# Kernel tuning notes

Hardware: AMD Instinct MI355X
Metric: run time of the kernel (lower is better)

Reference implementation:

```python
import jax, jax.numpy as jnp
import numpy as np
import math

D_MODEL = 1024
N_HEADS = 16
HEAD_DIM = D_MODEL // N_HEADS
PAD_INDEX = 0
NEG_INF = -1e9  # matches torch masked_fill value


def setup_inputs() -> dict:
    key = jax.random.key(0)
    ks = jax.random.split(key, 10)
    b, s = 2, 2048
    x = jax.random.normal(ks[0], (b, s, D_MODEL), dtype=jnp.float32)
    input_ids = jax.random.randint(ks[1], (b, s), 0, 32000, dtype=jnp.int64)
    scale = 1.0 / math.sqrt(D_MODEL)
    def lin(k):
        kw, kb = jax.random.split(k)
        W = jax.random.uniform(kw, (D_MODEL, D_MODEL), jnp.float32, -scale, scale)
        bb = jax.random.uniform(kb, (D_MODEL,), jnp.float32, -scale, scale)
        return W, bb
    Wq, bq = lin(ks[2])
    Wk, bk = lin(ks[3])
    Wv, bv = lin(ks[4])
    Wo, bo = lin(ks[5])
    return {"x": x, "input_ids": input_ids,
            "Wq": Wq, "bq": bq, "Wk": Wk, "bk": bk,
            "Wv": Wv, "bv": bv, "Wo": Wo, "bo": bo}


def reference(x, input_ids, Wq, bq, Wk, bk, Wv, bv, Wo, bo):
    b, s, _ = x.shape
    # torch nn.Linear: y = x @ W.T + b
    q = (x @ Wq.T + bq).reshape(b, s, N_HEADS, HEAD_DIM)
    k = (x @ Wk.T + bk).reshape(b, s, N_HEADS, HEAD_DIM)
    v = (x @ Wv.T + bv).reshape(b, s, N_HEADS, HEAD_DIM)
    # scores: [b, h, s, s]
    scores = jnp.einsum('bqhd,bkhd->bhqk', q, k) / math.sqrt(HEAD_DIM)
    pad_mask = (input_ids != PAD_INDEX)[:, None, None, :]          # [b,1,1,s] over keys
    causal = jnp.tril(jnp.ones((s, s), dtype=bool))[None, None]     # [1,1,s,s]
    final_mask = pad_mask & causal
    scores = jnp.where(final_mask, scores, NEG_INF)
    attn = jax.nn.softmax(scores, axis=-1)
    out = jnp.einsum('bhqk,bkhd->bqhd', attn, v).reshape(b, s, D_MODEL)
    return out @ Wo.T + bo
```

## Files before the change

kernel.cpp:

```cpp
#include <hip/hip_runtime.h>

#define DMODEL 1024
#define NHEADS 16
#define HDIM   64
#define BATCH  2
#define SEQ    2048
#define MROWS  (BATCH*SEQ)

typedef __bf16 bf16x8 __attribute__((ext_vector_type(8)));
typedef __bf16 bf16x4 __attribute__((ext_vector_type(4)));
typedef float floatx4 __attribute__((ext_vector_type(4)));

typedef const __attribute__((address_space(1))) void gvoid;
typedef __attribute__((address_space(3))) void lvoid;

template<bool V> struct ICb { static constexpr bool value = V; };

#define QSCALE 0.18033688011112042f

__global__ void cast_all(const float* __restrict__ x,
                         const float* __restrict__ wq, const float* __restrict__ wk,
                         const float* __restrict__ wv, const float* __restrict__ wo,
                         __bf16* __restrict__ xb, __bf16* __restrict__ wqb,
                         __bf16* __restrict__ wkb, __bf16* __restrict__ wvb,
                         __bf16* __restrict__ wob)
{
  const int u = blockIdx.x * 256 + threadIdx.x;
  const float* s; __bf16* o; int off;
  if (u < MROWS*DMODEL/8) { s = x; o = xb; off = u; }
  else {
    const int r = u - MROWS*DMODEL/8;
    const int w = r >> 17;
    off = r & 131071;
    s = (w == 0) ? wq : (w == 1) ? wk : (w == 2) ? wv : wo;
    o = (w == 0) ? wqb : (w == 1) ? wkb : (w == 2) ? wvb : wob;
  }
  const float4 f0 = ((const float4*)s)[off*2];
  const float4 f1 = ((const float4*)s)[off*2 + 1];
  bf16x8 v = {(__bf16)f0.x, (__bf16)f0.y, (__bf16)f0.z, (__bf16)f0.w,
              (__bf16)f1.x, (__bf16)f1.y, (__bf16)f1.z, (__bf16)f1.w};
  *(bf16x8*)(o + off*8) = v;
}

__global__ __launch_bounds__(256, 3)
void gemm_qkv(const unsigned short* __restrict__ A,
              const unsigned short* __restrict__ W0,
              const unsigned short* __restrict__ W1,
              const unsigned short* __restrict__ W2,
              const float* __restrict__ b0,
              const float* __restrict__ b1,
              const float* __restrict__ b2,
              unsigned short* __restrict__ qout,
              unsigned short* __restrict__ kout,
              unsigned short* __restrict__ vout)
{
  const int K = DMODEL;
  __shared__ unsigned short As[2][128*32];
  __shared__ unsigned short Bs[2][128*32];
  const int tid  = threadIdx.x;
  const int wid  = tid >> 6;
  const int lane = tid & 63;

  const int lin = blockIdx.x;
  const int wg  = (lin & 7)*96 + (lin >> 3);
  const int bx  = wg % 24;
  const int by  = wg / 24;
  const int brow = by * 128;
  const int bcol = bx * 128;
  const int wr = (wid >> 1) * 64;
  const int wc = (wid & 1) * 64;

  const int which = bcol >> 10;
  const unsigned short* Bw = which == 0 ? W0 : which == 1 ? W1 : W2;
  const float* bias = which == 0 ? b0 : which == 1 ? b1 : b2;
  const int bcolL = bcol & 1023;

  floatx4 acc[4][4] = {};

  const int sr = wid*16 + (lane >> 2);
  const int sc = (lane & 3) * 8;
  const int fr = lane & 15;
  const int fk = (lane >> 4) * 8;

#define GSTAGE(KT, B) do {                                                     \
    _Pragma("unroll")                                                          \
    for (int i_ = 0; i_ < 2; ++i_) {                                           \
      __builtin_amdgcn_global_load_lds(                                        \
          (gvoid*)(A + (size_t)(brow + i_*64 + sr)*K + (KT) + sc),             \
          (lvoid*)(As[B] + i_*2048 + wid*512), 16, 0, 0);                      \
      __builtin_amdgcn_global_load_lds(                                        \
          (gvoid*)(Bw + (size_t)(bcolL + i_*64 + sr)*K + (KT) + sc),           \
          (lvoid*)(Bs[B] + i_*2048 + wid*512), 16, 0, 0);                      \
    }                                                                          \
  } while (0)

  GSTAGE(0, 0);

  for (int kt = 0; kt < K; kt += 32) {
    const int cur = (kt >> 5) & 1;
    if (kt + 32 < K) {
      GSTAGE(kt + 32, cur ^ 1);
      asm volatile("s_waitcnt vmcnt(4)" ::: "memory");
    } else {
      asm volatile("s_waitcnt vmcnt(0)" ::: "memory");
    }
    __builtin_amdgcn_s_barrier();
    __builtin_amdgcn_sched_barrier(0);

    bf16x8 af[4], bfv[4];
#pragma unroll
    for (int m = 0; m < 4; ++m)
      af[m] = *(const bf16x8*)(As[cur] + (wr + m*16 + fr)*32 + fk);
#pragma unroll
    for (int n = 0; n < 4; ++n)
      bfv[n] = *(const bf16x8*)(Bs[cur] + (wc + n*16 + fr)*32 + fk);
    __builtin_amdgcn_s_setprio(1);
#pragma unroll
    for (int m = 0; m < 4; ++m)
#pragma unroll
      for (int n = 0; n < 4; ++n)
        acc[m][n] = __builtin_amdgcn_mfma_f32_16x16x32_bf16(af[m], bfv[n], acc[m][n], 0, 0, 0);
    __builtin_amdgcn_s_setprio(0);
    __builtin_amdgcn_s_barrier();
  }
#undef GSTAGE

  const int er = (lane >> 4) * 4;
  const int ec = lane & 15;
#pragma unroll
  for (int m = 0; m < 4; ++m) {
#pragma unroll
    for (int n = 0; n < 4; ++n) {
      const int colL = bcolL + wc + n*16 + ec;
      const float bv = bias[colL];
      const int rowb = brow + wr + m*16 + er;
      const int bi = rowb >> 11, s = rowb & 2047;
      const int hh = colL >> 6, dd = colL & 63;
      if (which == 2) {
        bf16x4 v4 = {(__bf16)(acc[m][n][0] + bv), (__bf16)(acc[m][n][1] + bv),
                     (__bf16)(acc[m][n][2] + bv), (__bf16)(acc[m][n][3] + bv)};
        *(bf16x4*)((__bf16*)vout + ((size_t)(bi*NHEADS + hh)*HDIM + dd)*SEQ + s) = v4;
      } else if (which == 0) {
        __bf16* o = (__bf16*)qout;
#pragma unroll
        for (int j = 0; j < 4; ++j)
          o[((size_t)(bi*NHEADS + hh)*SEQ + s + j)*HDIM + dd] =
              (__bf16)((acc[m][n][j] + bv) * QSCALE);
      } else {
        __bf16* o = (__bf16*)kout;
#pragma unroll
        for (int j = 0; j < 4; ++j)
          o[((size_t)(bi*NHEADS + hh)*SEQ + s + j)*HDIM + dd] = (__bf16)(acc[m][n][j] + bv);
      }
    }
  }
}

__global__ __launch_bounds__(256, 3)
void gemm_out(const unsigned short* __restrict__ A,
              const unsigned short* __restrict__ W,
              const float* __restrict__ bias,
              float* __restrict__ outf)
{
  const int K = DMODEL;
  __shared__ unsigned short As[2][128*64];
  __shared__ unsigned short Bs[2][64*64];
  const int tid  = threadIdx.x;
  const int wid  = tid >> 6;
  const int lane = tid & 63;

  const int lin = blockIdx.x;
  const int wg  = (lin & 7)*64 + (lin >> 3);
  const int bx  = wg & 15;
  const int by  = wg >> 4;
  const int brow = by * 128;
  const int bcol = bx * 64;
  const int wr = (wid >> 1) * 64;
  const int wc = (wid & 1) * 32;

  floatx4 acc[4][2] = {};

  const int fr  = lane & 15;
  const int hi4 = lane >> 4;

  const int r0 = tid >> 3;
  const int sw = ((tid & 7) ^ (r0 & 7)) * 8;

  auto gstage = [&](int kt, int B) {
#pragma unroll
    for (int i_ = 0; i_ < 4; ++i_)
      __builtin_amdgcn_global_load_lds(
          (gvoid*)(A + (size_t)(brow + i_*32 + r0)*K + kt + sw),
          (lvoid*)(As[B] + (i_*256 + tid)*8), 16, 0, 0);
#pragma unroll
    for (int i_ = 0; i_ < 2; ++i_)
      __builtin_amdgcn_global_load_lds(
          (gvoid*)(W + (size_t)(bcol + i_*32 + r0)*K + kt + sw),
          (lvoid*)(Bs[B] + (i_*256 + tid)*8), 16, 0, 0);
  };

  gstage(0, 0);

  for (int kt = 0; kt < K; kt += 64) {
    const int cur = (kt >> 6) & 1;
    if (kt + 64 < K) {
      gstage(kt + 64, cur ^ 1);
      asm volatile("s_waitcnt vmcnt(6)" ::: "memory");
    } else {
      asm volatile("s_waitcnt vmcnt(0)" ::: "memory");
    }
    __builtin_amdgcn_s_barrier();
    __builtin_amdgcn_sched_barrier(0);

    bf16x8 af[4][2], bfv[2][2];
#pragma unroll
    for (int m = 0; m < 4; ++m) {
      const int ra = wr + m*16 + fr;
#pragma unroll
      for (int c = 0; c < 2; ++c)
        af[m][c] = *(const bf16x8*)(As[cur] + ra*64 + (((c*4 + hi4) ^ (ra & 7)) * 8));
    }
#pragma unroll
    for (int n = 0; n < 2; ++n) {
      const int rb = wc + n*16 + fr;
#pragma unroll
      for (int c = 0; c < 2; ++c)
        bfv[n][c] = *(const bf16x8*)(Bs[cur] + rb*64 + (((c*4 + hi4) ^ (rb & 7)) * 8));
    }
    __builtin_amdgcn_s_setprio(1);
#pragma unroll
    for (int m = 0; m < 4; ++m)
#pragma unroll
      for (int n = 0; n < 2; ++n)
#pragma unroll
        for (int c = 0; c < 2; ++c)
          acc[m][n] = __builtin_amdgcn_mfma_f32_16x16x32_bf16(af[m][c], bfv[n][c], acc[m][n], 0, 0, 0);
    __builtin_amdgcn_s_setprio(0);
    __builtin_amdgcn_s_barrier();
  }

  const int er = hi4 * 4;
  const int ec = lane & 15;
#pragma unroll
  for (int m = 0; m < 4; ++m) {
#pragma unroll
    for (int n = 0; n < 2; ++n) {
      const int col = bcol + wc + n*16 + ec;
      const float bv = bias[col];
      const int rowb = brow + wr + m*16 + er;
#pragma unroll
      for (int j = 0; j < 4; ++j)
        outf[(size_t)(rowb + j)*DMODEL + col] = acc[m][n][j] + bv;
    }
  }
}

__global__ __launch_bounds__(512, 4)
void attn_fwd(const unsigned short* __restrict__ qb,
              const unsigned short* __restrict__ kb,
              const unsigned short* __restrict__ vtb,
              const int* __restrict__ ids,
              unsigned short* __restrict__ outb)
{
  const int hb = blockIdx.x;
  const int pr = blockIdx.y;
  const int h = hb & 15, bi = hb >> 4;

  const int tid = threadIdx.x, wid = tid >> 6, lane = tid & 63;
  const int grp  = wid >> 2;
  const int wid4 = wid & 3;
  const size_t hoff = (size_t)(bi*NHEADS + h) * SEQ * HDIM;
  const unsigned short* Qh  = qb  + hoff;
  const unsigned short* Kh  = kb  + hoff;
  const unsigned short* Vth = vtb + hoff;

  __shared__ unsigned short Ks[2][2][64*64];
  __shared__ unsigned short Vs[2][2][64*64];
  __shared__ unsigned short Ps[8][16*64];
  float* LOf = (float*)Ps;
  float* Ll  = (float*)Ks;

  const int q_   = lane & 15;
  const int hi4  = lane >> 4;
  const int koff = hi4 * 4;

  const int gt = tid & 255;
  const int r0 = gt >> 3;
  const int sw = ((gt & 7) ^ (r0 & 7)) * 8;
  unsigned short* Pw = Ps[wid];

#define STAGE(T, B) do {                                                       \
    const unsigned short* kbase_ = Kh + (size_t)((T)*64) * HDIM;               \
    const unsigned short* vbase_ = Vth + (T)*64;                               \
    __builtin_amdgcn_global_load_lds((gvoid*)(kbase_ + r0*64 + sw),            \
                                     (lvoid*)(Ks[grp][B] + gt*8), 16, 0, 0);   \
    __builtin_amdgcn_global_load_lds((gvoid*)(kbase_ + (r0+32)*64 + sw),       \
                                     (lvoid*)(Ks[grp][B] + (gt+256)*8), 16, 0, 0);\
    __builtin_amdgcn_global_load_lds((gvoid*)(vbase_ + (size_t)r0*SEQ + sw),   \
                                     (lvoid*)(Vs[grp][B] + gt*8), 16, 0, 0);   \
    __builtin_amdgcn_global_load_lds((gvoid*)(vbase_ + (size_t)(r0+32)*SEQ + sw),\
                                     (lvoid*)(Vs[grp][B] + (gt+256)*8), 16, 0, 0);\
  } while (0)

  for (int half = 0; half < 2; ++half) {
    const int qt = half ? 31 - pr : pr;
    const int qbase = qt * 64;
    const int qg = qbase + wid4*16 + q_;

    bf16x8 qf[2];
#pragma unroll
    for (int c = 0; c < 2; ++c)
      qf[c] = *(const bf16x8*)(Qh + (size_t)qg*HDIM + c*32 + hi4*8);

    float lsum = 0.f;
    floatx4 Oacc[4] = {};

    auto step = [&](auto Mc, int kb0, int bufc, unsigned long long wm) {
      constexpr bool MASKED = decltype(Mc)::value;

      floatx4 st[4];
      __builtin_amdgcn_s_setprio(1);
#pragma unroll
      for (int t = 0; t < 4; ++t) {
        st[t] = (floatx4){0.f, 0.f, 0.f, 0.f};
        const int kr = t*16 + q_;
#pragma unroll
        for (int c = 0; c < 2; ++c) {
          const int cd = ((c*4 + hi4) ^ (kr & 7)) * 8;
          bf16x8 kf = *(const bf16x8*)(Ks[grp][bufc] + kr*64 + cd);
          st[t] = __builtin_amdgcn_mfma_f32_16x16x32_bf16(kf, qf[c], st[t], 0, 0, 0);
        }
      }
      __builtin_amdgcn_s_setprio(0);

      float ps = 0.f;
#pragma unroll
      for (int t = 0; t < 4; ++t) {
        float p[4];
#pragma unroll
        for (int r = 0; r < 4; ++r) {
          float pv = exp2f(st[t][r]);
          if (MASKED) {
            const int ko = t*16 + koff + r;
            const bool dead = ((kb0 + ko) > qg) || (((wm >> ko) & 1ull) != 0ull);
            pv = dead ? 0.f : pv;
          }
          p[r] = pv;
          ps += pv;
        }
        bf16x4 pk = {(__bf16)p[0], (__bf16)p[1], (__bf16)p[2], (__bf16)p[3]};
        const int ko = t*16 + koff;
        *(bf16x4*)(Pw + q_*64 + (((ko >> 3) ^ (q_ & 7)) * 8) + (ko & 7)) = pk;
      }
      lsum += ps;

      __builtin_amdgcn_s_setprio(1);
#pragma unroll
      for (int cp = 0; cp < 2; ++cp) {
        const int ko = cp*32 + hi4*8;
        bf16x8 pf = *(const bf16x8*)(Pw + q_*64 + (((ko >> 3) ^ (q_ & 7)) * 8));
#pragma unroll
        for (int n = 0; n < 4; ++n) {
          const int d = n*16 + q_;
          const int cd = ((cp*4 + hi4) ^ (d & 7)) * 8;
          bf16x8 vf = *(const bf16x8*)(Vs[grp][bufc] + d*64 + cd);
          Oacc[n] = __builtin_amdgcn_mfma_f32_16x16x32_bf16(pf, vf, Oacc[n], 0, 0, 0);
        }
      }
      __builtin_amdgcn_s_setprio(0);
    };

    const int nT = qt + 1;
    const int h0 = (nT + 1) >> 1;
    const int cnt = (grp == 0) ? h0 : nT - h0;
    const int tb  = (grp == 0) ? 0 : h0;

    if (cnt > 0) STAGE(tb, 0);

    for (int i = 0; i < h0; ++i) {
      const bool valid = (i < cnt);
      const int t = tb + i;
      const int kb0 = t * 64;
      int pv = 1;
      if (valid) pv = ids[bi*SEQ + kb0 + lane];
      if (i + 1 < cnt) {
        STAGE(t + 1, (i + 1) & 1);
        asm volatile("s_waitcnt vmcnt(4)" ::: "memory");
      } else {
        asm volatile("s_waitcnt vmcnt(0)" ::: "memory");
      }
      const unsigned long long wm = __ballot(pv == 0);
      __builtin_amdgcn_s_barrier();
      __builtin_amdgcn_sched_barrier(0);

      if (valid) {
        const int bufc = i & 1;
        if ((t != nT - 1) && wm == 0ull) step(ICb<false>{}, kb0, bufc, 0ull);
        else                             step(ICb<true >{}, kb0, bufc, wm);
      }
      __builtin_amdgcn_s_barrier();
    }

    float lt = lsum + __shfl_xor(lsum, 16);
    lt += __shfl_xor(lt, 32);

    if (grp == 1) {
#pragma unroll
      for (int r = 0; r < 4; ++r)
#pragma unroll
        for (int n = 0; n < 4; ++n)
          LOf[(wid4*16 + koff + r)*64 + n*16 + q_] = Oacc[n][r];
      if (hi4 == 0) Ll[wid4*16 + q_] = lt;
    }
    __syncthreads();
    if (grp == 0) {
#pragma unroll
      for (int r = 0; r < 4; ++r) {
        const int rloc = wid4*16 + koff + r;
        const float inv = 1.f / (__shfl(lt, koff + r) + Ll[rloc]);
        const int row = bi*SEQ + qbase + rloc;
#pragma unroll
        for (int n = 0; n < 4; ++n) {
          const float o = Oacc[n][r] + LOf[rloc*64 + n*16 + q_];
          ((__bf16*)outb)[(size_t)row*DMODEL + h*HDIM + n*16 + q_] = (__bf16)(o * inv);
        }
      }
    }
    __syncthreads();
  }
#undef STAGE
}

extern "C" void kernel_launch(void* const* d_in, const int* in_sizes, int n_in,
                              void* d_out, int out_size, void* d_ws, size_t ws_size,
                              hipStream_t stream)
{
  const float* x  = (const float*)d_in[0];
  const int*   ids= (const int*)d_in[1];
  const float* Wq = (const float*)d_in[2];
  const float* bq = (const float*)d_in[3];
  const float* Wk = (const float*)d_in[4];
  const float* bk = (const float*)d_in[5];
  const float* Wv = (const float*)d_in[6];
  const float* bv = (const float*)d_in[7];
  const float* Wo = (const float*)d_in[8];
  const float* bo = (const float*)d_in[9];
  float* out = (float*)d_out;

  char* ws = (char*)d_ws;
  unsigned short* xb   = (unsigned short*)(ws);
  unsigned short* wqb  = (unsigned short*)(ws + ( 8u<<20));
  unsigned short* wkb  = (unsigned short*)(ws + (10u<<20));
  unsigned short* wvb  = (unsigned short*)(ws + (12u<<20));
  unsigned short* wob  = (unsigned short*)(ws + (14u<<20));
  unsigned short* qbuf = (unsigned short*)(ws + (16u<<20));
  unsigned short* kbuf = (unsigned short*)(ws + (24u<<20));
  unsigned short* vbuf = (unsigned short*)(ws + (32u<<20));
  unsigned short* abuf = (unsigned short*)(ws + (40u<<20));

  cast_all<<<4096, 256, 0, stream>>>(x, Wq, Wk, Wv, Wo,
                                     (__bf16*)xb, (__bf16*)wqb, (__bf16*)wkb,
                                     (__bf16*)wvb, (__bf16*)wob);

  gemm_qkv<<<768, 256, 0, stream>>>(xb, wqb, wkb, wvb, bq, bk, bv,
                                    qbuf, kbuf, vbuf);

  attn_fwd<<<dim3(32, 16), 512, 0, stream>>>(qbuf, kbuf, vbuf, ids, abuf);

  gemm_out<<<512, 256, 0, stream>>>(abuf, wob, bo, out);
}
```

Measured before the change: 105.4 us.

## Enlarge attention query tile to 128 rows, two 16-row subtiles per wave

The attention kernel now processes 128-query tiles (32 rows per wave, two MFMA subtiles sharing each K/V fragment load) instead of 64, halving the grid and doubling K/V reuse per LDS read. The two wave groups split the key range evenly (each takes qt+1 tiles), which replaces the earlier uneven split and its validity checks. The P scratch buffer doubles, and the final reduction reuses the K/V LDS buffers. The trade is more registers (launch bounds lowered to 2 blocks), fewer blocks in flight, and coarser causal masking.

```diff
diff --git a/kernel.cpp b/kernel.cpp
--- a/kernel.cpp
+++ b/kernel.cpp
@@ -13,8 +13,6 @@
 
 typedef const __attribute__((address_space(1))) void gvoid;
 typedef __attribute__((address_space(3))) void lvoid;
-
-template<bool V> struct ICb { static constexpr bool value = V; };
 
 #define QSCALE 0.18033688011112042f
 
@@ -255,7 +253,7 @@
   }
 }
 
-__global__ __launch_bounds__(512, 4)
+__global__ __launch_bounds__(512, 2)
 void attn_fwd(const unsigned short* __restrict__ qb,
               const unsigned short* __restrict__ kb,
               const unsigned short* __restrict__ vtb,
@@ -276,9 +274,9 @@
 
   __shared__ unsigned short Ks[2][2][64*64];
   __shared__ unsigned short Vs[2][2][64*64];
-  __shared__ unsigned short Ps[8][16*64];
-  float* LOf = (float*)Ps;
-  float* Ll  = (float*)Ks;
+  __shared__ unsigned short Ps[8][32*64];
+  float* LOf = (float*)Ks;
+  float* Ll  = (float*)Vs;
 
   const int q_   = lane & 15;
   const int hi4  = lane >> 4;
@@ -303,86 +301,29 @@
   } while (0)
 
   for (int half = 0; half < 2; ++half) {
-    const int qt = half ? 31 - pr : pr;
-    const int qbase = qt * 64;
-    const int qg = qbase + wid4*16 + q_;
-
-    bf16x8 qf[2];
-#pragma unroll
-    for (int c = 0; c < 2; ++c)
-      qf[c] = *(const bf16x8*)(Qh + (size_t)qg*HDIM + c*32 + hi4*8);
-
-    float lsum = 0.f;
-    floatx4 Oacc[4] = {};
-
-    auto step = [&](auto Mc, int kb0, int bufc, unsigned long long wm) {
-      constexpr bool MASKED = decltype(Mc)::value;
-
-      floatx4 st[4];
-      __builtin_amdgcn_s_setprio(1);
-#pragma unroll
-      for (int t = 0; t < 4; ++t) {
-        st[t] = (floatx4){0.f, 0.f, 0.f, 0.f};
-        const int kr = t*16 + q_;
-#pragma unroll
-        for (int c = 0; c < 2; ++c) {
-          const int cd = ((c*4 + hi4) ^ (kr & 7)) * 8;
-          bf16x8 kf = *(const bf16x8*)(Ks[grp][bufc] + kr*64 + cd);
-          st[t] = __builtin_amdgcn_mfma_f32_16x16x32_bf16(kf, qf[c], st[t], 0, 0, 0);
-        }
-      }
-      __builtin_amdgcn_s_setprio(0);
-
-      float ps = 0.f;
-#pragma unroll
-      for (int t = 0; t < 4; ++t) {
-        float p[4];
-#pragma unroll
-        for (int r = 0; r < 4; ++r) {
-          float pv = exp2f(st[t][r]);
-          if (MASKED) {
-            const int ko = t*16 + koff + r;
-            const bool dead = ((kb0 + ko) > qg) || (((wm >> ko) & 1ull) != 0ull);
-            pv = dead ? 0.f : pv;
-          }
-          p[r] = pv;
-          ps += pv;
-        }
-        bf16x4 pk = {(__bf16)p[0], (__bf16)p[1], (__bf16)p[2], (__bf16)p[3]};
-        const int ko = t*16 + koff;
-        *(bf16x4*)(Pw + q_*64 + (((ko >> 3) ^ (q_ & 7)) * 8) + (ko & 7)) = pk;
-      }
-      lsum += ps;
-
-      __builtin_amdgcn_s_setprio(1);
-#pragma unroll
-      for (int cp = 0; cp < 2; ++cp) {
-        const int ko = cp*32 + hi4*8;
-        bf16x8 pf = *(const bf16x8*)(Pw + q_*64 + (((ko >> 3) ^ (q_ & 7)) * 8));
-#pragma unroll
-        for (int n = 0; n < 4; ++n) {
-          const int d = n*16 + q_;
-          const int cd = ((cp*4 + hi4) ^ (d & 7)) * 8;
-          bf16x8 vf = *(const bf16x8*)(Vs[grp][bufc] + d*64 + cd);
-          Oacc[n] = __builtin_amdgcn_mfma_f32_16x16x32_bf16(pf, vf, Oacc[n], 0, 0, 0);
-        }
-      }
-      __builtin_amdgcn_s_setprio(0);
-    };
-
-    const int nT = qt + 1;
-    const int h0 = (nT + 1) >> 1;
-    const int cnt = (grp == 0) ? h0 : nT - h0;
-    const int tb  = (grp == 0) ? 0 : h0;
-
-    if (cnt > 0) STAGE(tb, 0);
-
-    for (int i = 0; i < h0; ++i) {
-      const bool valid = (i < cnt);
+    const int qt = half ? 15 - pr : pr;
+    const int qbase = qt * 128;
+    const int rowb = qbase + wid4*32;
+
+    bf16x8 qf[2][2];
+#pragma unroll
+    for (int s = 0; s < 2; ++s)
+#pragma unroll
+      for (int c = 0; c < 2; ++c)
+        qf[s][c] = *(const bf16x8*)(Qh + (size_t)(rowb + s*16 + q_)*HDIM + c*32 + hi4*8);
+
+    float lsum[2] = {0.f, 0.f};
+    floatx4 Oacc[2][4] = {};
+
+    const int cnt = qt + 1;
+    const int tb  = grp * cnt;
+
+    STAGE(tb, 0);
+
+    for (int i = 0; i < cnt; ++i) {
       const int t = tb + i;
       const int kb0 = t * 64;
-      int pv = 1;
-      if (valid) pv = ids[bi*SEQ + kb0 + lane];
+      const int pv = ids[bi*SEQ + kb0 + lane];
       if (i + 1 < cnt) {
         STAGE(t + 1, (i + 1) & 1);
         asm volatile("s_waitcnt vmcnt(4)" ::: "memory");
@@ -393,36 +334,102 @@
       __builtin_amdgcn_s_barrier();
       __builtin_amdgcn_sched_barrier(0);
 
-      if (valid) {
-        const int bufc = i & 1;
-        if ((t != nT - 1) && wm == 0ull) step(ICb<false>{}, kb0, bufc, 0ull);
-        else                             step(ICb<true >{}, kb0, bufc, wm);
-      }
+      const int bufc = i & 1;
+
+      floatx4 st[2][4];
+      __builtin_amdgcn_s_setprio(1);
+#pragma unroll
+      for (int t2 = 0; t2 < 4; ++t2) {
+        st[0][t2] = (floatx4){0.f, 0.f, 0.f, 0.f};
+        st[1][t2] = (floatx4){0.f, 0.f, 0.f, 0.f};
+        const int kr = t2*16 + q_;
+#pragma unroll
+        for (int c = 0; c < 2; ++c) {
+          const int cd = ((c*4 + hi4) ^ (kr & 7)) * 8;
+          bf16x8 kf = *(const bf16x8*)(Ks[grp][bufc] + kr*64 + cd);
+          st[0][t2] = __builtin_amdgcn_mfma_f32_16x16x32_bf16(kf, qf[0][c], st[0][t2], 0, 0, 0);
+          st[1][t2] = __builtin_amdgcn_mfma_f32_16x16x32_bf16(kf, qf[1][c], st[1][t2], 0, 0, 0);
+        }
+      }
+      __builtin_amdgcn_s_setprio(0);
+
+#pragma unroll
+      for (int s = 0; s < 2; ++s) {
+        const int qg = rowb + s*16 + q_;
+        const bool mk = (kb0 + 64 > rowb + s*16) || (wm != 0ull);
+        float ps = 0.f;
+#pragma unroll
+        for (int t2 = 0; t2 < 4; ++t2) {
+          float p[4];
+#pragma unroll
+          for (int r = 0; r < 4; ++r) {
+            float pvv = exp2f(st[s][t2][r]);
+            if (mk) {
+              const int ko = t2*16 + koff + r;
+              const bool dead = ((kb0 + ko) > qg) || (((wm >> ko) & 1ull) != 0ull);
+              pvv = dead ? 0.f : pvv;
+            }
+            p[r] = pvv;
+            ps += pvv;
+          }
+          bf16x4 pk = {(__bf16)p[0], (__bf16)p[1], (__bf16)p[2], (__bf16)p[3]};
+          const int ko = t2*16 + koff;
+          *(bf16x4*)(Pw + (s*16 + q_)*64 + (((ko >> 3) ^ (q_ & 7)) * 8) + (ko & 7)) = pk;
+        }
+        lsum[s] += ps;
+      }
+
+      __builtin_amdgcn_s_setprio(1);
+#pragma unroll
+      for (int cp = 0; cp < 2; ++cp) {
+        const int ko = cp*32 + hi4*8;
+        bf16x8 pf0 = *(const bf16x8*)(Pw + q_*64        + (((ko >> 3) ^ (q_ & 7)) * 8));
+        bf16x8 pf1 = *(const bf16x8*)(Pw + (16 + q_)*64 + (((ko >> 3) ^ (q_ & 7)) * 8));
+#pragma unroll
+        for (int n = 0; n < 4; ++n) {
+          const int d = n*16 + q_;
+          const int cd = ((cp*4 + hi4) ^ (d & 7)) * 8;
+          bf16x8 vf = *(const bf16x8*)(Vs[grp][bufc] + d*64 + cd);
+          Oacc[0][n] = __builtin_amdgcn_mfma_f32_16x16x32_bf16(pf0, vf, Oacc[0][n], 0, 0, 0);
+          Oacc[1][n] = __builtin_amdgcn_mfma_f32_16x16x32_bf16(pf1, vf, Oacc[1][n], 0, 0, 0);
+        }
+      }
+      __builtin_amdgcn_s_setprio(0);
       __builtin_amdgcn_s_barrier();
     }
 
-    float lt = lsum + __shfl_xor(lsum, 16);
-    lt += __shfl_xor(lt, 32);
+    float lt[2];
+#pragma unroll
+    for (int s = 0; s < 2; ++s) {
+      float v = lsum[s] + __shfl_xor(lsum[s], 16);
+      lt[s] = v + __shfl_xor(v, 32);
+    }
 
     if (grp == 1) {
 #pragma unroll
-      for (int r = 0; r < 4; ++r)
-#pragma unroll
-        for (int n = 0; n < 4; ++n)
-          LOf[(wid4*16 + koff + r)*64 + n*16 + q_] = Oacc[n][r];
-      if (hi4 == 0) Ll[wid4*16 + q_] = lt;
+      for (int s = 0; s < 2; ++s) {
+#pragma unroll
+        for (int r = 0; r < 4; ++r)
+#pragma unroll
+          for (int n = 0; n < 4; ++n)
+            LOf[(wid4*32 + s*16 + koff + r)*64 + n*16 + q_] = Oacc[s][n][r];
+        if (hi4 == 0) Ll[wid4*32 + s*16 + q_] = lt[s];
+      }
     }
     __syncthreads();
     if (grp == 0) {
 #pragma unroll
-      for (int r = 0; r < 4; ++r) {
-        const int rloc = wid4*16 + koff + r;
-        const float inv = 1.f / (__shfl(lt, koff + r) + Ll[rloc]);
-        const int row = bi*SEQ + qbase + rloc;
-#pragma unroll
-        for (int n = 0; n < 4; ++n) {
-          const float o = Oacc[n][r] + LOf[rloc*64 + n*16 + q_];
-          ((__bf16*)outb)[(size_t)row*DMODEL + h*HDIM + n*16 + q_] = (__bf16)(o * inv);
+      for (int s = 0; s < 2; ++s) {
+#pragma unroll
+        for (int r = 0; r < 4; ++r) {
+          const int rloc = wid4*32 + s*16 + koff + r;
+          const float inv = 1.f / (__shfl(lt[s], koff + r) + Ll[rloc]);
+          const int row = bi*SEQ + qbase + rloc;
+#pragma unroll
+          for (int n = 0; n < 4; ++n) {
+            const float o = Oacc[s][n][r] + LOf[rloc*64 + n*16 + q_];
+            ((__bf16*)outb)[(size_t)row*DMODEL + h*HDIM + n*16 + q_] = (__bf16)(o * inv);
+          }
         }
       }
     }
@@ -465,7 +472,7 @@
   gemm_qkv<<<768, 256, 0, stream>>>(xb, wqb, wkb, wvb, bq, bk, bv,
                                     qbuf, kbuf, vbuf);
 
-  attn_fwd<<<dim3(32, 16), 512, 0, stream>>>(qbuf, kbuf, vbuf, ids, abuf);
+  attn_fwd<<<dim3(32, 8), 512, 0, stream>>>(qbuf, kbuf, vbuf, ids, abuf);
 
   gemm_out<<<512, 256, 0, stream>>>(abuf, wob, bo, out);
 }
```

New measurement: 115.7 us. 1.1x slower.

## Restructure attention to 128-row query tiles with 32x32x16 MFMA

Applied to the files above, without the earlier changes.

The attention kernel now processes 128-query tiles per block, 32 rows per wave, using 32x32x16 bf16 MFMA instead of 16x16x32. Each block handles a single tile rather than a paired front/back half, and the two wave groups split the key range evenly. Tiles fully above the causal diagonal skip compute, and a single K buffer plus a double-buffered V buffer is used, loaded after a barrier. The aim is more operand reuse per LDS read and less loop overhead, at the cost of waiting on vmcnt(0) each iteration, which reduces load/compute overlap.

```diff
diff --git a/kernel.cpp b/kernel.cpp
--- a/kernel.cpp
+++ b/kernel.cpp
@@ -10,11 +10,10 @@
 typedef __bf16 bf16x8 __attribute__((ext_vector_type(8)));
 typedef __bf16 bf16x4 __attribute__((ext_vector_type(4)));
 typedef float floatx4 __attribute__((ext_vector_type(4)));
+typedef float floatx16 __attribute__((ext_vector_type(16)));
 
 typedef const __attribute__((address_space(1))) void gvoid;
 typedef __attribute__((address_space(3))) void lvoid;
-
-template<bool V> struct ICb { static constexpr bool value = V; };
 
 #define QSCALE 0.18033688011112042f
 
@@ -262,8 +261,10 @@
               const int* __restrict__ ids,
               unsigned short* __restrict__ outb)
 {
-  const int hb = blockIdx.x;
-  const int pr = blockIdx.y;
+  const int bx = blockIdx.x;
+  const int hb = bx & 31;
+  const int j  = (bx >> 5) & 7;
+  const int qt = (bx >> 8) ? 15 - j : j;
   const int h = hb & 15, bi = hb >> 4;
 
   const int tid = threadIdx.x, wid = tid >> 6, lane = tid & 63;
@@ -274,161 +275,155 @@
   const unsigned short* Kh  = kb  + hoff;
   const unsigned short* Vth = vtb + hoff;
 
-  __shared__ unsigned short Ks[2][2][64*64];
+  __shared__ unsigned short Ks[2][64*64];
   __shared__ unsigned short Vs[2][2][64*64];
-  __shared__ unsigned short Ps[8][16*64];
+  __shared__ unsigned short Ps[8][32*64];
   float* LOf = (float*)Ps;
   float* Ll  = (float*)Ks;
 
-  const int q_   = lane & 15;
-  const int hi4  = lane >> 4;
-  const int koff = hi4 * 4;
+  const int q32 = lane & 31;
+  const int hi2 = lane >> 5;
+  const int qbase = qt * 128;
+  const int rowb = qbase + wid4*32;
 
   const int gt = tid & 255;
   const int r0 = gt >> 3;
   const int sw = ((gt & 7) ^ (r0 & 7)) * 8;
   unsigned short* Pw = Ps[wid];
 
-#define STAGE(T, B) do {                                                       \
+#define STAGEK(T) do {                                                         \
     const unsigned short* kbase_ = Kh + (size_t)((T)*64) * HDIM;               \
+    __builtin_amdgcn_global_load_lds((gvoid*)(kbase_ + r0*64 + sw),            \
+                                     (lvoid*)(Ks[grp] + gt*8), 16, 0, 0);      \
+    __builtin_amdgcn_global_load_lds((gvoid*)(kbase_ + (r0+32)*64 + sw),       \
+                                     (lvoid*)(Ks[grp] + (gt+256)*8), 16, 0, 0);\
+  } while (0)
+#define STAGEV(T, B) do {                                                      \
     const unsigned short* vbase_ = Vth + (T)*64;                               \
-    __builtin_amdgcn_global_load_lds((gvoid*)(kbase_ + r0*64 + sw),            \
-                                     (lvoid*)(Ks[grp][B] + gt*8), 16, 0, 0);   \
-    __builtin_amdgcn_global_load_lds((gvoid*)(kbase_ + (r0+32)*64 + sw),       \
-                                     (lvoid*)(Ks[grp][B] + (gt+256)*8), 16, 0, 0);\
     __builtin_amdgcn_global_load_lds((gvoid*)(vbase_ + (size_t)r0*SEQ + sw),   \
                                      (lvoid*)(Vs[grp][B] + gt*8), 16, 0, 0);   \
     __builtin_amdgcn_global_load_lds((gvoid*)(vbase_ + (size_t)(r0+32)*SEQ + sw),\
                                      (lvoid*)(Vs[grp][B] + (gt+256)*8), 16, 0, 0);\
   } while (0)
 
-  for (int half = 0; half < 2; ++half) {
-    const int qt = half ? 31 - pr : pr;
-    const int qbase = qt * 64;
-    const int qg = qbase + wid4*16 + q_;
-
-    bf16x8 qf[2];
-#pragma unroll
-    for (int c = 0; c < 2; ++c)
-      qf[c] = *(const bf16x8*)(Qh + (size_t)qg*HDIM + c*32 + hi4*8);
-
-    float lsum = 0.f;
-    floatx4 Oacc[4] = {};
-
-    auto step = [&](auto Mc, int kb0, int bufc, unsigned long long wm) {
-      constexpr bool MASKED = decltype(Mc)::value;
-
-      floatx4 st[4];
-      __builtin_amdgcn_s_setprio(1);
-#pragma unroll
-      for (int t = 0; t < 4; ++t) {
-        st[t] = (floatx4){0.f, 0.f, 0.f, 0.f};
-        const int kr = t*16 + q_;
-#pragma unroll
-        for (int c = 0; c < 2; ++c) {
-          const int cd = ((c*4 + hi4) ^ (kr & 7)) * 8;
-          bf16x8 kf = *(const bf16x8*)(Ks[grp][bufc] + kr*64 + cd);
-          st[t] = __builtin_amdgcn_mfma_f32_16x16x32_bf16(kf, qf[c], st[t], 0, 0, 0);
+  bf16x8 qf[4];
+#pragma unroll
+  for (int s = 0; s < 4; ++s)
+    qf[s] = *(const bf16x8*)(Qh + (size_t)(rowb + q32)*HDIM + s*16 + hi2*8);
+
+  float lsum = 0.f;
+  floatx16 OA = {};
+  floatx16 OB = {};
+
+  const int cnt = qt + 1;
+  const int tb  = grp * cnt;
+
+  STAGEK(tb);
+  STAGEV(tb, 0);
+
+  for (int i = 0; i < cnt; ++i) {
+    const int t = tb + i;
+    const int kb0 = t * 64;
+    const int pv = ids[bi*SEQ + kb0 + lane];
+    asm volatile("s_waitcnt vmcnt(0)" ::: "memory");
+    const unsigned long long wm = __ballot(pv == 0);
+    __builtin_amdgcn_s_barrier();
+    __builtin_amdgcn_sched_barrier(0);
+
+    const int vbuf = i & 1;
+    const bool dead_all = (kb0 >= rowb + 32);
+    const bool masked = (kb0 + 63 > rowb) || (wm != 0ull);
+
+    if (!dead_all) {
+#pragma unroll
+      for (int kt2 = 0; kt2 < 2; ++kt2) {
+        floatx16 st = {};
+        const int krow = kt2*32 + q32;
+        __builtin_amdgcn_s_setprio(1);
+#pragma unroll
+        for (int s = 0; s < 4; ++s) {
+          bf16x8 kf = *(const bf16x8*)(Ks[grp] + krow*64 +
+                                       (((s*2 + hi2) ^ (krow & 7)) * 8));
+          st = __builtin_amdgcn_mfma_f32_32x32x16_bf16(kf, qf[s], st, 0, 0, 0);
+        }
+        __builtin_amdgcn_s_setprio(0);
+
+        float p[16];
+        if (!masked) {
+#pragma unroll
+          for (int r = 0; r < 16; ++r) { p[r] = exp2f(st[r]); lsum += p[r]; }
+        } else {
+          const int qg = rowb + q32;
+#pragma unroll
+          for (int r = 0; r < 16; ++r) {
+            const int crow = (r & 3) + 4*hi2 + 8*(r >> 2);
+            const int kl = kt2*32 + crow;
+            const bool dead = ((kb0 + kl) > qg) || (((wm >> kl) & 1ull) != 0ull);
+            p[r] = dead ? 0.f : exp2f(st[r]);
+            lsum += p[r];
+          }
+        }
+#pragma unroll
+        for (int g = 0; g < 4; ++g) {
+          bf16x4 pk = {(__bf16)p[g*4], (__bf16)p[g*4+1],
+                       (__bf16)p[g*4+2], (__bf16)p[g*4+3]};
+          const int c = kt2*4 + g;
+          *(bf16x4*)(Pw + q32*64 + ((c ^ (q32 & 7)) * 8) + hi2*4) = pk;
         }
       }
-      __builtin_amdgcn_s_setprio(0);
-
-      float ps = 0.f;
-#pragma unroll
-      for (int t = 0; t < 4; ++t) {
-        float p[4];
-#pragma unroll
-        for (int r = 0; r < 4; ++r) {
-          float pv = exp2f(st[t][r]);
-          if (MASKED) {
-            const int ko = t*16 + koff + r;
-            const bool dead = ((kb0 + ko) > qg) || (((wm >> ko) & 1ull) != 0ull);
-            pv = dead ? 0.f : pv;
-          }
-          p[r] = pv;
-          ps += pv;
-        }
-        bf16x4 pk = {(__bf16)p[0], (__bf16)p[1], (__bf16)p[2], (__bf16)p[3]};
-        const int ko = t*16 + koff;
-        *(bf16x4*)(Pw + q_*64 + (((ko >> 3) ^ (q_ & 7)) * 8) + (ko & 7)) = pk;
-      }
-      lsum += ps;
-
+    }
+    __builtin_amdgcn_s_barrier();
+
+    if (i + 1 < cnt) {
+      STAGEK(t + 1);
+      STAGEV(t + 1, vbuf ^ 1);
+    }
+
+    if (!dead_all) {
       __builtin_amdgcn_s_setprio(1);
 #pragma unroll
-      for (int cp = 0; cp < 2; ++cp) {
-        const int ko = cp*32 + hi4*8;
-        bf16x8 pf = *(const bf16x8*)(Pw + q_*64 + (((ko >> 3) ^ (q_ & 7)) * 8));
-#pragma unroll
-        for (int n = 0; n < 4; ++n) {
-          const int d = n*16 + q_;
-          const int cd = ((cp*4 + hi4) ^ (d & 7)) * 8;
-          bf16x8 vf = *(const bf16x8*)(Vs[grp][bufc] + d*64 + cd);
-          Oacc[n] = __builtin_amdgcn_mfma_f32_16x16x32_bf16(pf, vf, Oacc[n], 0, 0, 0);
-        }
+      for (int ks = 0; ks < 4; ++ks) {
+        const int ch = ((ks*2 + hi2) ^ (q32 & 7)) * 8;
+        bf16x8 pf  = *(const bf16x8*)(Pw + q32*64 + ch);
+        bf16x8 vf0 = *(const bf16x8*)(Vs[grp][vbuf] + q32*64 + ch);
+        bf16x8 vf1 = *(const bf16x8*)(Vs[grp][vbuf] + (32 + q32)*64 + ch);
+        OA = __builtin_amdgcn_mfma_f32_32x32x16_bf16(pf, vf0, OA, 0, 0, 0);
+        OB = __builtin_amdgcn_mfma_f32_32x32x16_bf16(pf, vf1, OB, 0, 0, 0);
       }
       __builtin_amdgcn_s_setprio(0);
-    };
-
-    const int nT = qt + 1;
-    const int h0 = (nT + 1) >> 1;
-    const int cnt = (grp == 0) ? h0 : nT - h0;
-    const int tb  = (grp == 0) ? 0 : h0;
-
-    if (cnt > 0) STAGE(tb, 0);
-
-    for (int i = 0; i < h0; ++i) {
-      const bool valid = (i < cnt);
-      const int t = tb + i;
-      const int kb0 = t * 64;
-      int pv = 1;
-      if (valid) pv = ids[bi*SEQ + kb0 + lane];
-      if (i + 1 < cnt) {
-        STAGE(t + 1, (i + 1) & 1);
-        asm volatile("s_waitcnt vmcnt(4)" ::: "memory");
-      } else {
-        asm volatile("s_waitcnt vmcnt(0)" ::: "memory");
-      }
-      const unsigned long long wm = __ballot(pv == 0);
-      __builtin_amdgcn_s_barrier();
-      __builtin_amdgcn_sched_barrier(0);
-
-      if (valid) {
-        const int bufc = i & 1;
-        if ((t != nT - 1) && wm == 0ull) step(ICb<false>{}, kb0, bufc, 0ull);
-        else                             step(ICb<true >{}, kb0, bufc, wm);
-      }
-      __builtin_amdgcn_s_barrier();
-    }
-
-    float lt = lsum + __shfl_xor(lsum, 16);
-    lt += __shfl_xor(lt, 32);
-
-    if (grp == 1) {
-#pragma unroll
-      for (int r = 0; r < 4; ++r)
-#pragma unroll
-        for (int n = 0; n < 4; ++n)
-          LOf[(wid4*16 + koff + r)*64 + n*16 + q_] = Oacc[n][r];
-      if (hi4 == 0) Ll[wid4*16 + q_] = lt;
-    }
-    __syncthreads();
-    if (grp == 0) {
-#pragma unroll
-      for (int r = 0; r < 4; ++r) {
-        const int rloc = wid4*16 + koff + r;
-        const float inv = 1.f / (__shfl(lt, koff + r) + Ll[rloc]);
-        const int row = bi*SEQ + qbase + rloc;
-#pragma unroll
-        for (int n = 0; n < 4; ++n) {
-          const float o = Oacc[n][r] + LOf[rloc*64 + n*16 + q_];
-          ((__bf16*)outb)[(size_t)row*DMODEL + h*HDIM + n*16 + q_] = (__bf16)(o * inv);
-        }
-      }
-    }
-    __syncthreads();
-  }
-#undef STAGE
+    }
+  }
+#undef STAGEK
+#undef STAGEV
+
+  float lt = lsum + __shfl_xor(lsum, 32);
+
+  __syncthreads();
+
+  if (grp == 1) {
+#pragma unroll
+    for (int r = 0; r < 16; ++r) {
+      const int crow = (r & 3) + 4*hi2 + 8*(r >> 2);
+      const int row = wid4*32 + crow;
+      LOf[row*64 + q32]      = OA[r];
+      LOf[row*64 + 32 + q32] = OB[r];
+    }
+    if (hi2 == 0) Ll[wid4*32 + q32] = lt;
+  }
+  __syncthreads();
+  if (grp == 0) {
+#pragma unroll
+    for (int r = 0; r < 16; ++r) {
+      const int crow = (r & 3) + 4*hi2 + 8*(r >> 2);
+      const int rloc = wid4*32 + crow;
+      const float inv = 1.f / (__shfl(lt, crow) + Ll[rloc]);
+      const size_t row = (size_t)(bi*SEQ + qbase + rloc);
+      const float o0 = OA[r] + LOf[rloc*64 + q32];
+      const float o1 = OB[r] + LOf[rloc*64 + 32 + q32];
+      ((__bf16*)outb)[row*DMODEL + h*HDIM + q32]      = (__bf16)(o0 * inv);
+      ((__bf16*)outb)[row*DMODEL + h*HDIM + 32 + q32] = (__bf16)(o1 * inv);
+    }
+  }
 }
 
 extern "C" void kernel_launch(void* const* d_in, const int* in_sizes, int n_in,
@@ -465,7 +460,7 @@
   gemm_qkv<<<768, 256, 0, stream>>>(xb, wqb, wkb, wvb, bq, bk, bv,
                                     qbuf, kbuf, vbuf);
 
-  attn_fwd<<<dim3(32, 16), 512, 0, stream>>>(qbuf, kbuf, vbuf, ids, abuf);
+  attn_fwd<<<512, 512, 0, stream>>>(qbuf, kbuf, vbuf, ids, abuf);
 
   gemm_out<<<512, 256, 0, stream>>>(abuf, wob, bo, out);
 }
```

Result: slower. 127.5 us (+21.0%).
